# Performance work log

Measured on AMD Instinct MI355X. Metric: run time of the kernel, lower is better.

Reference implementation:

```python
import jax, jax.numpy as jnp
import numpy as np

EPS = 1e-8
N_NODES, N_EDGES = 10000, 160000
SI, VI = 128, 16          # node scalar / vector channels
ES, EV = 32, 4            # edge scalar / vector channels
SO, VO = 128, 16          # output scalar / vector channels
MSI, MVI = 2 * SI + ES, 2 * VI + EV   # message input dims: 288, 36
H1 = max(MVI, VO)         # layer-1 hidden = 36 (bottleneck=1)
H2 = max(VO, VO)          # layer-2 hidden = 16
SVO = 3                   # scalarization_vectorization_output_dim


def _safe_norm(x, axis):
    return jnp.sqrt(jnp.sum(x * x, axis=axis) + EPS)


def _gcp(s, v, frames, Wdown, Wdf, Wso, bso, Wup, Wg, bg):
    """GCP block on edge-level inputs (node_inputs=False, vector_gate=True).
    s: [E, si], v: [E, vi, 3], frames: [E, 3, 3]."""
    v_pre = jnp.swapaxes(v, -1, -2)                 # [E, 3, vi]
    v_hid = v_pre @ Wdown                           # [E, 3, h]
    v_norm = _safe_norm(v_hid, axis=-2)             # [E, h]
    v_frames = v_pre @ Wdf                          # [E, 3, svo]
    # scalarize: frames @ v_frames -> [E,3,svo], transpose -> [E,svo,3], flatten to 9
    local = jnp.swapaxes(frames @ v_frames, -1, -2).reshape(v.shape[0], 3 * SVO)
    merged = jnp.concatenate([s, v_norm, local], axis=-1)
    s_out = merged @ Wso + bso                      # [E, so]
    v_out = jnp.swapaxes(v_hid @ Wup, -1, -2)       # [E, vo, 3]
    gate = jax.nn.sigmoid(jax.nn.silu(s_out) @ Wg + bg)  # vector gate
    v_out = v_out * gate[..., None]
    return jax.nn.silu(s_out), v_out


def _lin(key, fan_in, fan_out):
    return jax.random.normal(key, (fan_in, fan_out), dtype=jnp.float32) / np.sqrt(fan_in)


def setup_inputs() -> dict:
    key = jax.random.key(0)
    ks = jax.random.split(key, 24)
    M1 = H1 + MSI + 3 * SVO   # 333
    M2 = H2 + SO + 3 * SVO    # 153
    return {
        "node_s": jax.random.normal(ks[0], (N_NODES, SI), dtype=jnp.float32),
        "node_v": jax.random.normal(ks[1], (N_NODES, VI, 3), dtype=jnp.float32),
        "edge_s": jax.random.normal(ks[2], (N_EDGES, ES), dtype=jnp.float32),
        "edge_v": jax.random.normal(ks[3], (N_EDGES, EV, 3), dtype=jnp.float32),
        "frames": jax.random.normal(ks[4], (N_EDGES, 3, 3), dtype=jnp.float32),
        "g1_Wdown": _lin(ks[5], MVI, H1),
        "g1_Wdf": _lin(ks[6], MVI, SVO),
        "g1_Wso": _lin(ks[7], M1, SO),
        "g1_bso": jnp.zeros((SO,), dtype=jnp.float32),
        "g1_Wup": _lin(ks[8], H1, VO),
        "g1_Wg": _lin(ks[9], SO, VO),
        "g1_bg": jnp.zeros((VO,), dtype=jnp.float32),
        "g2_Wdown": _lin(ks[10], VO, H2),
        "g2_Wdf": _lin(ks[11], VO, SVO),
        "g2_Wso": _lin(ks[12], M2, SO),
        "g2_bso": jnp.zeros((SO,), dtype=jnp.float32),
        "g2_Wup": _lin(ks[13], H2, VO),
        "g2_Wg": _lin(ks[14], SO, VO),
        "g2_bg": jnp.zeros((VO,), dtype=jnp.float32),
        "att_W": _lin(ks[15], SO, 1),
        "att_b": jnp.zeros((1,), dtype=jnp.float32),
        "edge_index": jax.random.randint(ks[16], (2, N_EDGES), 0, N_NODES, dtype=jnp.int64),
    }


def reference(node_s, node_v, edge_s, edge_v, frames,
              g1_Wdown, g1_Wdf, g1_Wso, g1_bso, g1_Wup, g1_Wg, g1_bg,
              g2_Wdown, g2_Wdf, g2_Wso, g2_bso, g2_Wup, g2_Wg, g2_bg,
              att_W, att_b, edge_index):
    row, col = edge_index[0], edge_index[1]
    # edge gather: concat source node, edge, dest node features
    ms = jnp.concatenate([node_s[row], edge_s, node_s[col]], axis=-1)   # [E, 288]
    mv = jnp.concatenate([node_v[row], edge_v, node_v[col]], axis=1)    # [E, 36, 3]
    # message_fusion[0]
    s, v = _gcp(ms, mv, frames, g1_Wdown, g1_Wdf, g1_Wso, g1_bso, g1_Wup, g1_Wg, g1_bg)
    # message_fusion[1] with residual
    s2, v2 = _gcp(s, v, frames, g2_Wdown, g2_Wdf, g2_Wso, g2_bso, g2_Wup, g2_Wg, g2_bg)
    s, v = s + s2, v + v2
    # scalar message attention
    attn = jax.nn.sigmoid(s @ att_W + att_b)
    s = s * attn
    # flatten ScalarVector and scatter-sum aggregate to destination nodes
    flat = jnp.concatenate([s, v.reshape(v.shape[0], VO * 3)], axis=-1)  # [E, 176]
    agg = jax.ops.segment_sum(flat, row, num_segments=N_NODES)           # [N, 176]
    return agg
```

## Files before the change

### kernel.cpp

```cpp
#include <hip/hip_runtime.h>
#include <hip/hip_bf16.h>

#define E_TOT 160000
#define NN    10000
#define EPB   32

typedef unsigned short ushortT;
typedef unsigned int   uintT;
typedef __attribute__((ext_vector_type(8))) short short8;
typedef __attribute__((ext_vector_type(4))) float f32x4;

__device__ __forceinline__ float sigmoidf_(float x) { return 1.0f / (1.0f + __expf(-x)); }
__device__ __forceinline__ float siluf_(float x) { return x * sigmoidf_(x); }

__device__ __forceinline__ ushortT f2b(float f) {
    union { float f; uintT u; } x; x.f = f;
    uintT r = x.u + 0x7fffu + ((x.u >> 16) & 1u);
    return (ushortT)(r >> 16);
}
__device__ __forceinline__ float b2f(ushortT h) {
    union { uintT u; float f; } x; x.u = ((uintT)h) << 16; return x.f;
}
__device__ __forceinline__ uintT pk2(float lo, float hi) {
    union { __hip_bfloat162 h; uintT u; } cv;
    cv.h = __float22bfloat162_rn(make_float2(lo, hi));
    return cv.u;
}
__device__ __forceinline__ short8 ldfrag(const float* p) {
    const float4 x = ((const float4*)p)[0];
    const float4 y = ((const float4*)p)[1];
    union { uintT u[4]; short8 s; } r;
    r.u[0] = pk2(x.x, x.y); r.u[1] = pk2(x.z, x.w);
    r.u[2] = pk2(y.x, y.y); r.u[3] = pk2(y.z, y.w);
    return r.s;
}

#define OFF_W1SO 0
#define OFF_W2SO 45056
#define OFF_W1DF 65536
#define OFF_W1G  68608
#define OFF_W1UP 70656
#define OFF_W2DF 71680
#define OFF_W2G  72704
#define OFF_W2UP 74752
#define WT_USH   75264

#define NOFF_OFF   56320000ULL
#define CUR_OFF    56360016ULL
#define WT_OFF     57040032ULL
#define WS_CSR     57190560ULL
#define NS16_OFF   57190560ULL
#define WS_NS      59750560ULL
#define PR_OFF     59750560ULL
#define PC_OFF     62310560ULL
#define PRE_END    64870560ULL

__device__ __forceinline__ bool idx_is64(const int* pi) {
    return (pi[1] | pi[3] | pi[5] | pi[7] | pi[9] | pi[11] | pi[13] | pi[15]) == 0;
}

__device__ __forceinline__ void weight_prep(
    int i,
    const float* __restrict__ W1so, const float* __restrict__ W2so,
    const float* __restrict__ W1d,  const float* __restrict__ W1f,
    const float* __restrict__ W1g,  const float* __restrict__ W1up,
    const float* __restrict__ W2d,  const float* __restrict__ W2f,
    const float* __restrict__ W2g,  const float* __restrict__ W2up,
    ushortT* __restrict__ ws)
{
    if (i < OFF_W2SO) {
        int n = i / 352, k = i - n * 352;
        ws[i] = (k < 333) ? f2b(W1so[k * 128 + n]) : (ushortT)0;
    } else if (i < OFF_W1DF) {
        int j = i - OFF_W2SO, n = j / 160, k = j - n * 160;
        ws[i] = (k < 153) ? f2b(W2so[k * 128 + n]) : (ushortT)0;
    } else if (i < OFF_W1G) {
        int j = i - OFF_W1DF, n = j / 64, k = j - n * 64;
        float v = 0.f;
        if (k < 36) { if (n < 36) v = W1d[k * 36 + n]; else if (n < 39) v = W1f[k * 3 + (n - 36)]; }
        ws[i] = f2b(v);
    } else if (i < OFF_W1UP) {
        int j = i - OFF_W1G, n = j / 128, k = j - n * 128;
        ws[i] = f2b(W1g[k * 16 + n]);
    } else if (i < OFF_W2DF) {
        int j = i - OFF_W1UP, n = j / 64, k = j - n * 64;
        ws[i] = (k < 36) ? f2b(W1up[k * 16 + n]) : (ushortT)0;
    } else if (i < OFF_W2G) {
        int j = i - OFF_W2DF, n = j / 32, k = j - n * 32;
        float v = 0.f;
        if (k < 16) { if (n < 16) v = W2d[k * 16 + n]; else if (n < 19) v = W2f[k * 3 + (n - 16)]; }
        ws[i] = f2b(v);
    } else if (i < OFF_W2UP) {
        int j = i - OFF_W2G, n = j / 128, k = j - n * 128;
        ws[i] = f2b(W2g[k * 16 + n]);
    } else if (i < WT_USH) {
        int j = i - OFF_W2UP, n = j / 32, k = j - n * 32;
        ws[i] = (k < 16) ? f2b(W2up[k * 16 + n]) : (ushortT)0;
    }
}

__global__ __launch_bounds__(256) void setup_kernel(
    const float* __restrict__ W1so, const float* __restrict__ W2so,
    const float* __restrict__ W1d,  const float* __restrict__ W1f,
    const float* __restrict__ W1g,  const float* __restrict__ W1up,
    const float* __restrict__ W2d,  const float* __restrict__ W2f,
    const float* __restrict__ W2g,  const float* __restrict__ W2up,
    ushortT* __restrict__ ws,
    const void* __restrict__ eidx, int* __restrict__ cur,
    const float* __restrict__ node_s,
    ushortT* __restrict__ ns16)
{
    int i = blockIdx.x * 256 + threadIdx.x;
    {
        const int* pi = (const int*)eidx;
        const long long* pl = (const long long*)eidx;
        int r = idx_is64(pi) ? (int)pl[i] : pi[i];
        atomicAdd(&cur[r], 1);
    }
    if (ns16 && i < 160000) {
        float4 x = ((const float4*)node_s)[i * 2];
        float4 y = ((const float4*)node_s)[i * 2 + 1];
        uint4 st;
        st.x = pk2(x.x, x.y); st.y = pk2(x.z, x.w);
        st.z = pk2(y.x, y.y); st.w = pk2(y.z, y.w);
        ((uint4*)ns16)[i] = st;
    }
    weight_prep(i, W1so, W2so, W1d, W1f, W1g, W1up, W2d, W2f, W2g, W2up, ws);
}

__global__ __launch_bounds__(256) void prep_kernel(
    const float* __restrict__ W1so, const float* __restrict__ W2so,
    const float* __restrict__ W1d,  const float* __restrict__ W1f,
    const float* __restrict__ W1g,  const float* __restrict__ W1up,
    const float* __restrict__ W2d,  const float* __restrict__ W2f,
    const float* __restrict__ W2g,  const float* __restrict__ W2up,
    ushortT* __restrict__ ws, float* __restrict__ out)
{
    int i = blockIdx.x * 256 + threadIdx.x;
    float4* o4 = (float4*)out;
    #pragma unroll
    for (int k = 0; k < 6; ++k) {
        int z = i + k * 75264;
        if (z < 440000) o4[z] = make_float4(0.f, 0.f, 0.f, 0.f);
    }
    weight_prep(i, W1so, W2so, W1d, W1f, W1g, W1up, W2d, W2f, W2g, W2up, ws);
}

__global__ __launch_bounds__(256) void scan_kernel(int* __restrict__ cur,
                                                   int* __restrict__ noff)
{
    __shared__ int buf[10000];
    __shared__ int partial[256];
    const int t = threadIdx.x;
    for (int i = t; i < NN; i += 256) buf[i] = cur[i];
    for (int i = t; i < NN; i += 256) cur[i] = 0;
    __syncthreads();
    const int base = t * 40;
    int s = 0;
    #pragma unroll
    for (int i = 0; i < 40; ++i) s += (base + i < NN) ? buf[base + i] : 0;
    partial[t] = s;
    __syncthreads();
    for (int o = 1; o < 256; o <<= 1) {
        int v = (t >= o) ? partial[t - o] : 0;
        __syncthreads();
        partial[t] += v;
        __syncthreads();
    }
    int run = (t == 0) ? 0 : partial[t - 1];
    #pragma unroll
    for (int i = 0; i < 40; ++i) {
        int gi = base + i;
        if (gi < NN) { int v = buf[gi]; noff[gi] = run; run += v; }
    }
    if (t == 255) noff[NN] = partial[255];
}

#define MFMA(a, b, c) __builtin_amdgcn_mfma_f32_16x16x32_bf16((a), (b), (c), 0, 0, 0)

__global__ __launch_bounds__(256) void pre_kernel(
    const ushortT* __restrict__ ns16, const ushortT* __restrict__ wt,
    ushortT* __restrict__ prt, ushortT* __restrict__ pct,
    int* __restrict__ cur, int* __restrict__ noff)
{
    __shared__ int sbuf[10000];
    __shared__ int spart[256];
    const int t = threadIdx.x;
    if (blockIdx.x == 625) {
        for (int i = t; i < NN; i += 256) sbuf[i] = cur[i];
        for (int i = t; i < NN; i += 256) cur[i] = 0;
        __syncthreads();
        const int base = t * 40;
        int s = 0;
        #pragma unroll
        for (int i = 0; i < 40; ++i) s += (base + i < NN) ? sbuf[base + i] : 0;
        spart[t] = s;
        __syncthreads();
        for (int o = 1; o < 256; o <<= 1) {
            int v = (t >= o) ? spart[t - o] : 0;
            __syncthreads();
            spart[t] += v;
            __syncthreads();
        }
        int run = (t == 0) ? 0 : spart[t - 1];
        #pragma unroll
        for (int i = 0; i < 40; ++i) {
            int gi = base + i;
            if (gi < NN) { int v = sbuf[gi]; noff[gi] = run; run += v; }
        }
        if (t == 255) noff[NN] = spart[255];
        return;
    }
    const int w = t >> 6, lane = t & 63, lq = lane >> 4, ln = lane & 15, klq = lq * 8;
    const int nb = blockIdx.x * 16;
    const int dn0 = w * 32 + ln, dn1 = dn0 + 16;
    const ushortT* b0p = wt + dn0 * 352 + klq;
    const ushortT* b1p = wt + dn1 * 352 + klq;
    const ushortT* arow = ns16 + (size_t)(nb + ln) * 128 + klq;
    f32x4 a00 = {0,0,0,0}, a01 = {0,0,0,0}, a10 = {0,0,0,0}, a11 = {0,0,0,0};
    #pragma unroll
    for (int ks = 0; ks < 4; ++ks) {
        short8 a  = *(const short8*)(arow + ks * 32);
        short8 b0 = *(const short8*)(b0p + ks * 32);
        short8 b1 = *(const short8*)(b1p + ks * 32);
        short8 c0 = *(const short8*)(b0p + 160 + ks * 32);
        short8 c1 = *(const short8*)(b1p + 160 + ks * 32);
        a00 = MFMA(a, b0, a00); a01 = MFMA(a, b1, a01);
        a10 = MFMA(a, c0, a10); a11 = MFMA(a, c1, a11);
    }
    #pragma unroll
    for (int r = 0; r < 4; ++r) {
        int n = nb + lq * 4 + r;
        prt[(size_t)n * 128 + dn0] = f2b(a00[r]);
        prt[(size_t)n * 128 + dn1] = f2b(a01[r]);
        pct[(size_t)n * 128 + dn0] = f2b(a10[r]);
        pct[(size_t)n * 128 + dn1] = f2b(a11[r]);
    }
}

__global__ __launch_bounds__(256) void node_kernel(const ushortT* __restrict__ fb,
                                                   const int* __restrict__ noff,
                                                   float* __restrict__ out)
{
    const int w = threadIdx.x >> 6, l = threadIdx.x & 63;
    const int n = blockIdx.x * 4 + w;
    if (l >= 44) return;
    const int s = noff[n], eend = noff[n + 1];
    float a0 = 0.f, a1 = 0.f, a2 = 0.f, a3 = 0.f;
    int idx = s;
    for (; idx + 2 <= eend; idx += 2) {
        uint2 p0 = *(const uint2*)(fb + (size_t)idx * 176 + l * 4);
        uint2 p1 = *(const uint2*)(fb + (size_t)(idx + 1) * 176 + l * 4);
        a0 += b2f((ushortT)(p0.x & 0xffff)); a1 += b2f((ushortT)(p0.x >> 16));
        a2 += b2f((ushortT)(p0.y & 0xffff)); a3 += b2f((ushortT)(p0.y >> 16));
        a0 += b2f((ushortT)(p1.x & 0xffff)); a1 += b2f((ushortT)(p1.x >> 16));
        a2 += b2f((ushortT)(p1.y & 0xffff)); a3 += b2f((ushortT)(p1.y >> 16));
    }
    if (idx < eend) {
        uint2 p0 = *(const uint2*)(fb + (size_t)idx * 176 + l * 4);
        a0 += b2f((ushortT)(p0.x & 0xffff)); a1 += b2f((ushortT)(p0.x >> 16));
        a2 += b2f((ushortT)(p0.y & 0xffff)); a3 += b2f((ushortT)(p0.y >> 16));
    }
    ((float4*)(out + (size_t)n * 176))[l] = make_float4(a0, a1, a2, a3);
}

__global__ __launch_bounds__(256, 6) void edge_kernel(
    const float* __restrict__ node_s, const float* __restrict__ node_v,
    const float* __restrict__ edge_s, const float* __restrict__ edge_v,
    const float* __restrict__ frames,
    const float* __restrict__ b1so, const float* __restrict__ b1g,
    const float* __restrict__ b2so, const float* __restrict__ b2g,
    const float* __restrict__ attW, const float* __restrict__ attb,
    const ushortT* __restrict__ wsc,
    const void* __restrict__ eidx, float* __restrict__ out,
    ushortT* __restrict__ fb, int* __restrict__ cur, const int* __restrict__ noff,
    const ushortT* __restrict__ ns16,
    const ushortT* __restrict__ prt, const ushortT* __restrict__ pct,
    int csr)
{
    const ushortT* W1T   = wsc + OFF_W1SO;
    const ushortT* W2T   = wsc + OFF_W2SO;
    const ushortT* W1dfT = wsc + OFF_W1DF;
    const ushortT* W1gT  = wsc + OFF_W1G;
    const ushortT* W1upT = wsc + OFF_W1UP;
    const ushortT* W2dfT = wsc + OFF_W2DF;
    const ushortT* W2gT  = wsc + OFF_W2G;
    const ushortT* W2upT = wsc + OFF_W2UP;

    __shared__ __align__(16) char smem[27136];
    ushortT* mvA     = (ushortT*)smem;
    ushortT* m2      = (ushortT*)smem;
    ushortT* vhidA   = (ushortT*)(smem + 10752);
    ushortT* s2s     = (ushortT*)(smem + 10752);
    ushortT* normbuf = (ushortT*)(smem + 19456);
    ushortT* v1s     = (ushortT*)(smem + 19456);
    ushortT* vhid2A  = (ushortT*)(smem + 19456);
    float*   fr      = (float*)(smem + 24064);
    float*   vfr2f   = (float*)(smem + 25216);
    ushortT* v1f     = (ushortT*)(smem + 24064);

    const int t  = threadIdx.x;
    const int eg = blockIdx.x * EPB;
    const int w  = t >> 6, lane = t & 63, lq = lane >> 4, ln = lane & 15;
    const int te = t >> 3, tj = t & 7;
    const int p  = w & 1;

    const int* pi = (const int*)eidx;
    const long long* pl = (const long long*)eidx;
    const bool is64 = idx_is64(pi);

    int posr = 0;
    float att_reg = 0.f;

    const int nrT = is64 ? (int)pl[eg + te] : pi[eg + te];
    const int ncT = is64 ? (int)pl[E_TOT + eg + te] : pi[E_TOT + eg + te];

    uint4 pga = {0,0,0,0}, pgb = {0,0,0,0}, pgc = {0,0,0,0}, pgd = {0,0,0,0};
    {
        #pragma unroll
        for (int mi = 0; mi < 2; ++mi) {
            if (mi == 1 && tj != 0) break;
            int m = (mi == 0) ? tj : 8;
            const float* src;
            if (m < 4)       src = node_v + nrT * 48 + 12 * m;
            else if (m == 4) src = edge_v + (eg + te) * 12;
            else             src = node_v + ncT * 48 + 12 * (m - 5);
            float4 x = ((const float4*)src)[0];
            float4 y = ((const float4*)src)[1];
            float4 z = ((const float4*)src)[2];
            float v[12] = {x.x, x.y, x.z, x.w, y.x, y.y, y.z, y.w, z.x, z.y, z.z, z.w};
            int c0 = 4 * m;
            #pragma unroll
            for (int sp = 0; sp < 3; ++sp) {
                *(uintT*)(mvA + (sp * 32 + te) * 40 + c0)     = pk2(v[sp],     v[3 + sp]);
                *(uintT*)(mvA + (sp * 32 + te) * 40 + c0 + 2) = pk2(v[6 + sp], v[9 + sp]);
            }
        }
        if (prt) {
            const ushortT* pr_ = prt + (size_t)nrT * 128 + tj * 16;
            const ushortT* pc_ = pct + (size_t)ncT * 128 + tj * 16;
            pga = ((const uint4*)pr_)[0]; pgb = ((const uint4*)pr_)[1];
            pgc = ((const uint4*)pc_)[0]; pgd = ((const uint4*)pc_)[1];
        }
        #pragma unroll
        for (int k = 0; k < 2; ++k) {
            int j = tj + k * 8;
            if (j < 9) fr[te * 9 + j] = frames[(eg + te) * 9 + j];
        }
        #pragma unroll
        for (int k = 0; k < 3; ++k) {
            int c = 45 + tj + k * 8;
            if (c < 64) normbuf[te * 72 + c] = 0;
        }
        if (t < 192) {
            int r = t >> 1, cc = 36 + ((t & 1) << 1);
            *(uintT*)(mvA + r * 40 + cc) = 0;
        }
        if (csr && tj == 0) {
            posr = noff[nrT] + atomicAdd(&cur[nrT], 1);
        }
    }

    const int klq = lq * 8;
    const int dn0 = w * 32 + ln, dn1 = dn0 + 16;
    const ushortT* b0p = W1T + dn0 * 352 + klq;
    const ushortT* b1p = W1T + dn1 * 352 + klq;
    f32x4 acc00 = {0,0,0,0}, acc01 = {0,0,0,0}, acc10 = {0,0,0,0}, acc11 = {0,0,0,0};
    float dbi0, dbi1;
    {
        const int e0 = ln, e1 = 16 + ln;
        const int eb0 = (eg + e0) * 32, eb1 = (eg + e1) * 32;
        dbi0 = b1so[dn0]; dbi1 = b1so[dn1];
        if (prt) {
            short8 a0 = ldfrag(edge_s + eb0 + klq);
            short8 a1 = ldfrag(edge_s + eb1 + klq);
            short8 b0 = *(const short8*)(b0p + 128);
            short8 b1 = *(const short8*)(b1p + 128);
            acc00 = MFMA(a0, b0, acc00); acc01 = MFMA(a0, b1, acc01);
            acc10 = MFMA(a1, b0, acc10); acc11 = MFMA(a1, b1, acc11);
        } else {
            int r0, c0, r1, c1;
            if (is64) {
                r0 = (int)pl[eg + e0]; r1 = (int)pl[eg + e1];
                c0 = (int)pl[E_TOT + eg + e0]; c1 = (int)pl[E_TOT + eg + e1];
            } else {
                r0 = pi[eg + e0]; r1 = pi[eg + e1];
                c0 = pi[E_TOT + eg + e0]; c1 = pi[E_TOT + eg + e1];
            }
            r0 *= 128; c0 *= 128; r1 *= 128; c1 *= 128;
            #pragma unroll
            for (int ks = 0; ks < 9; ++ks) {
                short8 a0, a1;
                if (ks < 4) {
                    if (ns16) {
                        a0 = *(const short8*)(ns16 + r0 + ks * 32 + klq);
                        a1 = *(const short8*)(ns16 + r1 + ks * 32 + klq);
                    } else {
                        a0 = ldfrag(node_s + r0 + ks * 32 + klq);
                        a1 = ldfrag(node_s + r1 + ks * 32 + klq);
                    }
                } else if (ks == 4) {
                    a0 = ldfrag(edge_s + eb0 + klq);
                    a1 = ldfrag(edge_s + eb1 + klq);
                } else {
                    if (ns16) {
                        a0 = *(const short8*)(ns16 + c0 + (ks - 5) * 32 + klq);
                        a1 = *(const short8*)(ns16 + c1 + (ks - 5) * 32 + klq);
                    } else {
                        a0 = ldfrag(node_s + c0 + (ks - 5) * 32 + klq);
                        a1 = ldfrag(node_s + c1 + (ks - 5) * 32 + klq);
                    }
                }
                short8 b0 = *(const short8*)(b0p + ks * 32);
                short8 b1 = *(const short8*)(b1p + ks * 32);
                acc00 = MFMA(a0, b0, acc00); acc01 = MFMA(a0, b1, acc01);
                acc10 = MFMA(a1, b0, acc10); acc11 = MFMA(a1, b1, acc11);
            }
        }
    }
    asm volatile("" : "+v"(acc00), "+v"(acc01), "+v"(acc10), "+v"(acc11));
    __syncthreads();

    for (int u = w; u < 18; u += 4) {
        int mt = u / 3, nt = u - mt * 3;
        const ushortT* ap = mvA + (mt * 16 + ln) * 40 + lq * 8;
        const ushortT* bp = W1dfT + (nt * 16 + ln) * 64 + lq * 8;
        f32x4 acc = {0.f, 0.f, 0.f, 0.f};
        acc = MFMA(*(const short8*)ap, *(const short8*)bp, acc);
        short8 a2 = {0, 0, 0, 0, 0, 0, 0, 0};
        if (lq == 0) a2 = *(const short8*)(ap + 32);
        acc = MFMA(a2, *(const short8*)(bp + 32), acc);
        if (nt < 2 || ln < 8) {
            ushortT* op = vhidA + (mt * 16 + lq * 4) * 40 + nt * 16 + ln;
            op[0]   = f2b(acc[0]); op[40]  = f2b(acc[1]);
            op[80]  = f2b(acc[2]); op[120] = f2b(acc[3]);
        }
    }
    __syncthreads();

    {
        #pragma unroll
        for (int k = 0; k < 5; ++k) {
            int h = tj + k * 8;
            if (h < 36) {
                float a0 = b2f(vhidA[te * 40 + h]);
                float a1 = b2f(vhidA[(32 + te) * 40 + h]);
                float a2 = b2f(vhidA[(64 + te) * 40 + h]);
                normbuf[te * 72 + h] = f2b(sqrtf(fmaf(a0, a0, fmaf(a1, a1, fmaf(a2, a2, 1e-8f)))));
            }
        }
        for (int i = t; i < 288; i += 256) {
            int e = i / 9, r = i - e * 9, a = r / 3, b = r - a * 3;
            float x = fr[e * 9 + b * 3 + 0] * b2f(vhidA[e * 40 + 36 + a])
                    + fr[e * 9 + b * 3 + 1] * b2f(vhidA[(32 + e) * 40 + 36 + a])
                    + fr[e * 9 + b * 3 + 2] * b2f(vhidA[(64 + e) * 40 + 36 + a]);
            normbuf[e * 72 + 36 + r] = f2b(x);
        }
        if (prt) {
            uintT pr_[8] = {pga.x, pga.y, pga.z, pga.w, pgb.x, pgb.y, pgb.z, pgb.w};
            uintT pc_[8] = {pgc.x, pgc.y, pgc.z, pgc.w, pgd.x, pgd.y, pgd.z, pgd.w};
            uintT* dst = (uintT*)(m2 + te * 168 + tj * 16);
            #pragma unroll
            for (int j = 0; j < 8; ++j) {
                float lo = b2f((ushortT)(pr_[j] & 0xffff)) + b2f((ushortT)(pc_[j] & 0xffff));
                float hi = b2f((ushortT)(pr_[j] >> 16))    + b2f((ushortT)(pc_[j] >> 16));
                dst[j] = pk2(lo, hi);
            }
        }
    }
    __syncthreads();

    {
        const int e0 = ln, e1 = 16 + ln;
        #pragma unroll
        for (int ks = 9; ks < 11; ++ks) {
            short8 a0 = *(const short8*)(normbuf + e0 * 72 + (ks - 9) * 32 + klq);
            short8 a1 = *(const short8*)(normbuf + e1 * 72 + (ks - 9) * 32 + klq);
            short8 b0 = *(const short8*)(b0p + ks * 32);
            short8 b1 = *(const short8*)(b1p + ks * 32);
            acc00 = MFMA(a0, b0, acc00); acc01 = MFMA(a0, b1, acc01);
            acc10 = MFMA(a1, b0, acc10); acc11 = MFMA(a1, b1, acc11);
        }
        if (prt) {
            #pragma unroll
            for (int r = 0; r < 4; ++r) {
                int m0 = lq * 4 + r;
                float p00 = b2f(m2[m0 * 168 + dn0]);
                float p01 = b2f(m2[m0 * 168 + dn1]);
                float p10 = b2f(m2[(16 + m0) * 168 + dn0]);
                float p11 = b2f(m2[(16 + m0) * 168 + dn1]);
                m2[m0 * 168 + dn0]        = f2b(siluf_(acc00[r] + p00 + dbi0));
                m2[m0 * 168 + dn1]        = f2b(siluf_(acc01[r] + p01 + dbi1));
                m2[(16 + m0) * 168 + dn0] = f2b(siluf_(acc10[r] + p10 + dbi0));
                m2[(16 + m0) * 168 + dn1] = f2b(siluf_(acc11[r] + p11 + dbi1));
            }
        } else {
            #pragma unroll
            for (int r = 0; r < 4; ++r) {
                int m0 = lq * 4 + r;
                m2[m0 * 168 + dn0]        = f2b(siluf_(acc00[r] + dbi0));
                m2[m0 * 168 + dn1]        = f2b(siluf_(acc01[r] + dbi1));
                m2[(16 + m0) * 168 + dn0] = f2b(siluf_(acc10[r] + dbi0));
                m2[(16 + m0) * 168 + dn1] = f2b(siluf_(acc11[r] + dbi1));
            }
        }
    }
    __syncthreads();

    float v1reg[2][4] = {{0.f,0.f,0.f,0.f},{0.f,0.f,0.f,0.f}};
    {
        f32x4 gacc = {0,0,0,0};
        {
            const ushortT* ap = m2 + (p * 16 + ln) * 168;
            const ushortT* bp = W1gT + ln * 128;
            #pragma unroll
            for (int ks = 0; ks < 4; ++ks)
                gacc = MFMA(*(const short8*)(ap + ks * 32 + lq * 8),
                            *(const short8*)(bp + ks * 32 + lq * 8), gacc);
        }
        float g1[4];
        {
            float bi = b1g[ln];
            #pragma unroll
            for (int r = 0; r < 4; ++r) g1[r] = sigmoidf_(gacc[r] + bi);
        }
        const ushortT* bpu = W1upT + ln * 64 + lq * 8;
        short8 bu1 = *(const short8*)bpu;
        short8 bu2 = *(const short8*)(bpu + 32);
        #pragma unroll
        for (int c = 0; c < 2; ++c) {
            if (c == 1 && w >= 2) break;
            int mt = w + c * 4;
            const ushortT* ap = vhidA + (mt * 16 + ln) * 40 + lq * 8;
            f32x4 acc = {0,0,0,0};
            acc = MFMA(*(const short8*)ap, bu1, acc);
            short8 a2 = {0, 0, 0, 0, 0, 0, 0, 0};
            if (lq == 0) a2 = *(const short8*)(ap + 32);
            acc = MFMA(a2, bu2, acc);
            #pragma unroll
            for (int r = 0; r < 4; ++r) {
                int row = mt * 16 + lq * 4 + r;
                float vv = acc[r] * g1[r];
                v1reg[c][r] = vv;
                v1s[row * 16 + ln] = f2b(vv);
            }
        }
        #pragma unroll
        for (int c = 0; c < 2; ++c) {
            if (c == 1 && w >= 2) break;
            int mt = w + c * 4;
            const ushortT* ap = v1s + (mt * 16 + ln) * 16 + lq * 8;
            short8 a = {0, 0, 0, 0, 0, 0, 0, 0};
            if (lq < 2) a = *(const short8*)ap;
            #pragma unroll
            for (int nt = 0; nt < 2; ++nt) {
                const ushortT* bp = W2dfT + (nt * 16 + ln) * 32 + lq * 8;
                f32x4 acc = {0,0,0,0};
                acc = MFMA(a, *(const short8*)bp, acc);
                if (nt == 0) {
                    ushortT* op = vhid2A + (mt * 16 + lq * 4) * 16 + ln;
                    op[0]  = f2b(acc[0]); op[16] = f2b(acc[1]);
                    op[32] = f2b(acc[2]); op[48] = f2b(acc[3]);
                } else if (ln < 3) {
                    float* op = vfr2f + (mt * 16 + lq * 4) * 3 + ln;
                    op[0] = acc[0]; op[3] = acc[1]; op[6] = acc[2]; op[9] = acc[3];
                }
            }
        }
    }
    __syncthreads();

    {
        #pragma unroll
        for (int k = 0; k < 2; ++k) {
            int i = t + k * 256, e = i >> 4, h = i & 15;
            float a0 = b2f(vhid2A[e * 16 + h]);
            float a1 = b2f(vhid2A[(32 + e) * 16 + h]);
            float a2 = b2f(vhid2A[(64 + e) * 16 + h]);
            m2[e * 168 + 128 + h] = f2b(sqrtf(fmaf(a0, a0, fmaf(a1, a1, fmaf(a2, a2, 1e-8f)))));
        }
        for (int i = t; i < 288; i += 256) {
            int e = i / 9, r = i - e * 9, a = r / 3, b = r - a * 3;
            float x = fr[e * 9 + b * 3 + 0] * vfr2f[e * 3 + a]
                    + fr[e * 9 + b * 3 + 1] * vfr2f[(32 + e) * 3 + a]
                    + fr[e * 9 + b * 3 + 2] * vfr2f[(64 + e) * 3 + a];
            m2[e * 168 + 144 + r] = f2b(x);
        }
        if (tj) m2[te * 168 + 152 + tj] = 0;
    }
    __syncthreads();

    {
        f32x4 acc00i = {0,0,0,0}, acc01i = {0,0,0,0}, acc10i = {0,0,0,0}, acc11i = {0,0,0,0};
        const ushortT* a0p = m2 + ln * 168 + lq * 8;
        const ushortT* a1p = m2 + (16 + ln) * 168 + lq * 8;
        const ushortT* b0pi = W2T + (w * 32 + ln) * 160 + lq * 8;
        const ushortT* b1pi = W2T + (w * 32 + 16 + ln) * 160 + lq * 8;
        #pragma unroll
        for (int ks = 0; ks < 5; ++ks) {
            short8 a0 = *(const short8*)(a0p + ks * 32);
            short8 a1 = *(const short8*)(a1p + ks * 32);
            short8 b0 = *(const short8*)(b0pi + ks * 32);
            short8 b1 = *(const short8*)(b1pi + ks * 32);
            acc00i = MFMA(a0, b0, acc00i); acc01i = MFMA(a0, b1, acc01i);
            acc10i = MFMA(a1, b0, acc10i); acc11i = MFMA(a1, b1, acc11i);
        }
        const int n0 = w * 32 + ln, n1 = n0 + 16;
        float bi0 = b2so[n0], bi1 = b2so[n1];
        #pragma unroll
        for (int r = 0; r < 4; ++r) {
            int m0 = lq * 4 + r;
            s2s[m0 * 136 + n0]        = f2b(siluf_(acc00i[r] + bi0));
            s2s[m0 * 136 + n1]        = f2b(siluf_(acc01i[r] + bi1));
            s2s[(16 + m0) * 136 + n0] = f2b(siluf_(acc10i[r] + bi0));
            s2s[(16 + m0) * 136 + n1] = f2b(siluf_(acc11i[r] + bi1));
        }
    }
    __syncthreads();

    {
        f32x4 gacc = {0,0,0,0};
        {
            const ushortT* ap = s2s + (p * 16 + ln) * 136;
            const ushortT* bp = W2gT + ln * 128;
            #pragma unroll
            for (int ks = 0; ks < 4; ++ks)
                gacc = MFMA(*(const short8*)(ap + ks * 32 + lq * 8),
                            *(const short8*)(bp + ks * 32 + lq * 8), gacc);
        }
        float g2[4];
        {
            float bi = b2g[ln];
            #pragma unroll
            for (int r = 0; r < 4; ++r) g2[r] = sigmoidf_(gacc[r] + bi);
        }
        const ushortT* bpu = W2upT + ln * 32 + lq * 8;
        short8 bu = *(const short8*)bpu;
        #pragma unroll
        for (int c = 0; c < 2; ++c) {
            if (c == 1 && w >= 2) break;
            int mt = w + c * 4;
            const ushortT* ap = vhid2A + (mt * 16 + ln) * 16 + lq * 8;
            short8 a = {0, 0, 0, 0, 0, 0, 0, 0};
            if (lq < 2) a = *(const short8*)ap;
            f32x4 acc = {0,0,0,0};
            acc = MFMA(a, bu, acc);
            #pragma unroll
            for (int r = 0; r < 4; ++r) {
                int row = mt * 16 + lq * 4 + r;
                float vfin = v1reg[c][r] + acc[r] * g2[r];
                v1f[row * 16 + ln] = f2b(vfin);
            }
        }
        {
            float sum = 0.f;
            int c0 = tj * 16;
            #pragma unroll
            for (int c = c0; c < c0 + 16; ++c)
                sum = fmaf(b2f(m2[te * 168 + c]) + b2f(s2s[te * 136 + c]), attW[c], sum);
            sum += __shfl_xor(sum, 4);
            sum += __shfl_xor(sum, 2);
            sum += __shfl_xor(sum, 1);
            att_reg = sigmoidf_(sum + attb[0]);
        }
    }
    __syncthreads();

    {
        const float at = att_reg;
        if (csr) {
            const int pos = __shfl(posr, lane & 56);
            ushortT* fbe = fb + (size_t)pos * 176;
            #pragma unroll
            for (int k = 0; k < 11; ++k) {
                int j = 2 * tj + 16 * k;
                float v0, v1;
                if (j < 128) {
                    v0 = (b2f(m2[te * 168 + j])     + b2f(s2s[te * 136 + j]))     * at;
                    v1 = (b2f(m2[te * 168 + j + 1]) + b2f(s2s[te * 136 + j + 1])) * at;
                } else {
                    int r = j - 128;
                    int o0 = r / 3,        sp0 = r - o0 * 3;
                    int o1 = (r + 1) / 3,  sp1 = (r + 1) - o1 * 3;
                    v0 = b2f(v1f[(sp0 * 32 + te) * 16 + o0]);
                    v1 = b2f(v1f[(sp1 * 32 + te) * 16 + o1]);
                }
                *(uintT*)(fbe + j) = pk2(v0, v1);
            }
        } else {
            const int orow = nrT * 176;
            #pragma unroll
            for (int k = 0; k < 22; ++k) {
                int j = tj + k * 8;
                float val;
                if (j < 128) {
                    val = (b2f(m2[te * 168 + j]) + b2f(s2s[te * 136 + j])) * at;
                } else {
                    int r = j - 128, o = r / 3, sp = r - o * 3;
                    val = b2f(v1f[(sp * 32 + te) * 16 + o]);
                }
                atomicAdd(&out[orow + j], val);
            }
        }
    }
}

extern "C" void kernel_launch(void* const* d_in, const int* in_sizes, int n_in,
                              void* d_out, int out_size, void* d_ws, size_t ws_size,
                              hipStream_t stream) {
    const float* node_s = (const float*)d_in[0];
    const float* node_v = (const float*)d_in[1];
    const float* edge_s = (const float*)d_in[2];
    const float* edge_v = (const float*)d_in[3];
    const float* frames = (const float*)d_in[4];
    const float* W1d  = (const float*)d_in[5];
    const float* W1f  = (const float*)d_in[6];
    const float* W1so = (const float*)d_in[7];
    const float* b1so = (const float*)d_in[8];
    const float* W1up = (const float*)d_in[9];
    const float* W1g  = (const float*)d_in[10];
    const float* b1g  = (const float*)d_in[11];
    const float* W2d  = (const float*)d_in[12];
    const float* W2f  = (const float*)d_in[13];
    const float* W2so = (const float*)d_in[14];
    const float* b2so = (const float*)d_in[15];
    const float* W2up = (const float*)d_in[16];
    const float* W2g  = (const float*)d_in[17];
    const float* b2g  = (const float*)d_in[18];
    const float* attW = (const float*)d_in[19];
    const float* attb = (const float*)d_in[20];
    const void*  eidx = d_in[21];

    float* out = (float*)d_out;
    char* ws = (char*)d_ws;

    const int csr = ws_size >= WS_CSR;
    ushortT* wt    = csr ? (ushortT*)(ws + WT_OFF)  : (ushortT*)ws;
    ushortT* fbuf  = csr ? (ushortT*)ws             : nullptr;
    int*     noff  = csr ? (int*)(ws + NOFF_OFF)    : nullptr;
    int*     cur   = csr ? (int*)(ws + CUR_OFF)     : nullptr;
    ushortT* ns16  = (ws_size >= WS_NS) ? (ushortT*)(ws + NS16_OFF) : nullptr;
    const int pre  = csr && ns16 && (ws_size >= PRE_END);
    ushortT* prt   = pre ? (ushortT*)(ws + PR_OFF) : nullptr;
    ushortT* pct   = pre ? (ushortT*)(ws + PC_OFF) : nullptr;

    if (csr) {
        hipMemsetAsync(cur, 0, NN * sizeof(int), stream);
        setup_kernel<<<625, 256, 0, stream>>>(
            W1so, W2so, W1d, W1f, W1g, W1up, W2d, W2f, W2g, W2up,
            wt, eidx, cur, node_s, ns16);
        if (pre) {
            pre_kernel<<<626, 256, 0, stream>>>(ns16, wt, prt, pct, cur, noff);
        } else {
            scan_kernel<<<1, 256, 0, stream>>>(cur, noff);
        }
    } else {
        prep_kernel<<<294, 256, 0, stream>>>(W1so, W2so, W1d, W1f, W1g, W1up,
                                             W2d, W2f, W2g, W2up, wt, out);
    }

    edge_kernel<<<E_TOT / EPB, 256, 0, stream>>>(
        node_s, node_v, edge_s, edge_v, frames,
        b1so, b1g, b2so, b2g, attW, attb,
        (const ushortT*)wt, eidx, out, fbuf, cur, noff, ns16, prt, pct, csr);

    if (csr) {
        node_kernel<<<2500, 256, 0, stream>>>((const ushortT*)fbuf, noff, out);
    }
}
```

Baseline: 277.8 us.

## Fold node pre-projection into setup kernel and drop bf16 node copy

The per-node projection of node_s through the W1so row and column blocks now runs in extra blocks of setup_kernel. Those blocks load node_s fp32 directly and stage a swizzled bf16 weight tile in shared memory, so the separate ns16 conversion buffer and pre_kernel launch go away. The scan moves back to its own single-block kernel. Separately, node_kernel's gather loop is unrolled from 2 to 4 edges. This trades one launch and an intermediate buffer for per-block weight staging in the setup blocks and a serial scan launch.

```diff
diff --git a/kernel.cpp b/kernel.cpp
--- a/kernel.cpp
+++ b/kernel.cpp
@@ -49,11 +49,9 @@
 #define CUR_OFF    56360016ULL
 #define WT_OFF     57040032ULL
 #define WS_CSR     57190560ULL
-#define NS16_OFF   57190560ULL
-#define WS_NS      59750560ULL
-#define PR_OFF     59750560ULL
-#define PC_OFF     62310560ULL
-#define PRE_END    64870560ULL
+#define PR_OFF     57190560ULL
+#define PC_OFF     59750560ULL
+#define PRE_END    62310560ULL
 
 __device__ __forceinline__ bool idx_is64(const int* pi) {
     return (pi[1] | pi[3] | pi[5] | pi[7] | pi[9] | pi[11] | pi[13] | pi[15]) == 0;
@@ -99,6 +97,8 @@
     }
 }
 
+#define MFMA(a, b, c) __builtin_amdgcn_mfma_f32_16x16x32_bf16((a), (b), (c), 0, 0, 0)
+
 __global__ __launch_bounds__(256) void setup_kernel(
     const float* __restrict__ W1so, const float* __restrict__ W2so,
     const float* __restrict__ W1d,  const float* __restrict__ W1f,
@@ -108,22 +108,58 @@
     ushortT* __restrict__ ws,
     const void* __restrict__ eidx, int* __restrict__ cur,
     const float* __restrict__ node_s,
-    ushortT* __restrict__ ns16)
+    ushortT* __restrict__ prt, ushortT* __restrict__ pct)
 {
-    int i = blockIdx.x * 256 + threadIdx.x;
+    __shared__ __align__(16) ushortT wtile[128 * 128];
+    const int t = threadIdx.x;
+
+    if (blockIdx.x >= 625) {
+        if (!prt) return;
+        const int nb = (blockIdx.x - 625) * 64;
+        const int w = t >> 6, lane = t & 63, lq = lane >> 4, ln = lane & 15, klq = lq * 8;
+        int arow = nb + w * 16 + ln;
+        if (arow > NN - 1) arow = NN - 1;
+        short8 af[4];
+        #pragma unroll
+        for (int ks = 0; ks < 4; ++ks)
+            af[ks] = ldfrag(node_s + (size_t)arow * 128 + ks * 32 + klq);
+        const int n_ = t & 127, half = t >> 7, nsw8 = n_ & 7;
+        for (int pass = 0; pass < 2; ++pass) {
+            const int base = pass ? 160 : 0;
+            for (int kk = 0; kk < 64; ++kk) {
+                int kt = kk * 2 + half;
+                float v = W1so[(base + kt) * 128 + n_];
+                wtile[n_ * 128 + ((((kt >> 3) ^ nsw8) << 3) | (kt & 7))] = f2b(v);
+            }
+            __syncthreads();
+            ushortT* dst = pass ? pct : prt;
+            #pragma unroll
+            for (int ct = 0; ct < 8; ++ct) {
+                f32x4 ar = {0, 0, 0, 0};
+                const int n = ct * 16 + ln, nsw = n & 7;
+                #pragma unroll
+                for (int ks = 0; ks < 4; ++ks) {
+                    const int kb = ks * 32 + klq;
+                    const short8 br = *(const short8*)(wtile + n * 128 + (((kb >> 3) ^ nsw) << 3));
+                    ar = MFMA(af[ks], br, ar);
+                }
+                #pragma unroll
+                for (int r = 0; r < 4; ++r) {
+                    const int node = nb + w * 16 + lq * 4 + r;
+                    if (node < NN) dst[(size_t)node * 128 + ct * 16 + ln] = f2b(ar[r]);
+                }
+            }
+            __syncthreads();
+        }
+        return;
+    }
+
+    int i = blockIdx.x * 256 + t;
     {
         const int* pi = (const int*)eidx;
         const long long* pl = (const long long*)eidx;
         int r = idx_is64(pi) ? (int)pl[i] : pi[i];
         atomicAdd(&cur[r], 1);
-    }
-    if (ns16 && i < 160000) {
-        float4 x = ((const float4*)node_s)[i * 2];
-        float4 y = ((const float4*)node_s)[i * 2 + 1];
-        uint4 st;
-        st.x = pk2(x.x, x.y); st.y = pk2(x.z, x.w);
-        st.z = pk2(y.x, y.y); st.w = pk2(y.z, y.w);
-        ((uint4*)ns16)[i] = st;
     }
     weight_prep(i, W1so, W2so, W1d, W1f, W1g, W1up, W2d, W2f, W2g, W2up, ws);
 }
@@ -176,68 +212,6 @@
     if (t == 255) noff[NN] = partial[255];
 }
 
-#define MFMA(a, b, c) __builtin_amdgcn_mfma_f32_16x16x32_bf16((a), (b), (c), 0, 0, 0)
-
-__global__ __launch_bounds__(256) void pre_kernel(
-    const ushortT* __restrict__ ns16, const ushortT* __restrict__ wt,
-    ushortT* __restrict__ prt, ushortT* __restrict__ pct,
-    int* __restrict__ cur, int* __restrict__ noff)
-{
-    __shared__ int sbuf[10000];
-    __shared__ int spart[256];
-    const int t = threadIdx.x;
-    if (blockIdx.x == 625) {
-        for (int i = t; i < NN; i += 256) sbuf[i] = cur[i];
-        for (int i = t; i < NN; i += 256) cur[i] = 0;
-        __syncthreads();
-        const int base = t * 40;
-        int s = 0;
-        #pragma unroll
-        for (int i = 0; i < 40; ++i) s += (base + i < NN) ? sbuf[base + i] : 0;
-        spart[t] = s;
-        __syncthreads();
-        for (int o = 1; o < 256; o <<= 1) {
-            int v = (t >= o) ? spart[t - o] : 0;
-            __syncthreads();
-            spart[t] += v;
-            __syncthreads();
-        }
-        int run = (t == 0) ? 0 : spart[t - 1];
-        #pragma unroll
-        for (int i = 0; i < 40; ++i) {
-            int gi = base + i;
-            if (gi < NN) { int v = sbuf[gi]; noff[gi] = run; run += v; }
-        }
-        if (t == 255) noff[NN] = spart[255];
-        return;
-    }
-    const int w = t >> 6, lane = t & 63, lq = lane >> 4, ln = lane & 15, klq = lq * 8;
-    const int nb = blockIdx.x * 16;
-    const int dn0 = w * 32 + ln, dn1 = dn0 + 16;
-    const ushortT* b0p = wt + dn0 * 352 + klq;
-    const ushortT* b1p = wt + dn1 * 352 + klq;
-    const ushortT* arow = ns16 + (size_t)(nb + ln) * 128 + klq;
-    f32x4 a00 = {0,0,0,0}, a01 = {0,0,0,0}, a10 = {0,0,0,0}, a11 = {0,0,0,0};
-    #pragma unroll
-    for (int ks = 0; ks < 4; ++ks) {
-        short8 a  = *(const short8*)(arow + ks * 32);
-        short8 b0 = *(const short8*)(b0p + ks * 32);
-        short8 b1 = *(const short8*)(b1p + ks * 32);
-        short8 c0 = *(const short8*)(b0p + 160 + ks * 32);
-        short8 c1 = *(const short8*)(b1p + 160 + ks * 32);
-        a00 = MFMA(a, b0, a00); a01 = MFMA(a, b1, a01);
-        a10 = MFMA(a, c0, a10); a11 = MFMA(a, c1, a11);
-    }
-    #pragma unroll
-    for (int r = 0; r < 4; ++r) {
-        int n = nb + lq * 4 + r;
-        prt[(size_t)n * 128 + dn0] = f2b(a00[r]);
-        prt[(size_t)n * 128 + dn1] = f2b(a01[r]);
-        pct[(size_t)n * 128 + dn0] = f2b(a10[r]);
-        pct[(size_t)n * 128 + dn1] = f2b(a11[r]);
-    }
-}
-
 __global__ __launch_bounds__(256) void node_kernel(const ushortT* __restrict__ fb,
                                                    const int* __restrict__ noff,
                                                    float* __restrict__ out)
@@ -248,15 +222,21 @@
     const int s = noff[n], eend = noff[n + 1];
     float a0 = 0.f, a1 = 0.f, a2 = 0.f, a3 = 0.f;
     int idx = s;
-    for (; idx + 2 <= eend; idx += 2) {
+    for (; idx + 4 <= eend; idx += 4) {
         uint2 p0 = *(const uint2*)(fb + (size_t)idx * 176 + l * 4);
         uint2 p1 = *(const uint2*)(fb + (size_t)(idx + 1) * 176 + l * 4);
+        uint2 p2 = *(const uint2*)(fb + (size_t)(idx + 2) * 176 + l * 4);
+        uint2 p3 = *(const uint2*)(fb + (size_t)(idx + 3) * 176 + l * 4);
         a0 += b2f((ushortT)(p0.x & 0xffff)); a1 += b2f((ushortT)(p0.x >> 16));
         a2 += b2f((ushortT)(p0.y & 0xffff)); a3 += b2f((ushortT)(p0.y >> 16));
         a0 += b2f((ushortT)(p1.x & 0xffff)); a1 += b2f((ushortT)(p1.x >> 16));
         a2 += b2f((ushortT)(p1.y & 0xffff)); a3 += b2f((ushortT)(p1.y >> 16));
-    }
-    if (idx < eend) {
+        a0 += b2f((ushortT)(p2.x & 0xffff)); a1 += b2f((ushortT)(p2.x >> 16));
+        a2 += b2f((ushortT)(p2.y & 0xffff)); a3 += b2f((ushortT)(p2.y >> 16));
+        a0 += b2f((ushortT)(p3.x & 0xffff)); a1 += b2f((ushortT)(p3.x >> 16));
+        a2 += b2f((ushortT)(p3.y & 0xffff)); a3 += b2f((ushortT)(p3.y >> 16));
+    }
+    for (; idx < eend; ++idx) {
         uint2 p0 = *(const uint2*)(fb + (size_t)idx * 176 + l * 4);
         a0 += b2f((ushortT)(p0.x & 0xffff)); a1 += b2f((ushortT)(p0.x >> 16));
         a2 += b2f((ushortT)(p0.y & 0xffff)); a3 += b2f((ushortT)(p0.y >> 16));
@@ -392,24 +372,14 @@
             for (int ks = 0; ks < 9; ++ks) {
                 short8 a0, a1;
                 if (ks < 4) {
-                    if (ns16) {
-                        a0 = *(const short8*)(ns16 + r0 + ks * 32 + klq);
-                        a1 = *(const short8*)(ns16 + r1 + ks * 32 + klq);
-                    } else {
-                        a0 = ldfrag(node_s + r0 + ks * 32 + klq);
-                        a1 = ldfrag(node_s + r1 + ks * 32 + klq);
-                    }
+                    a0 = ldfrag(node_s + r0 + ks * 32 + klq);
+                    a1 = ldfrag(node_s + r1 + ks * 32 + klq);
                 } else if (ks == 4) {
                     a0 = ldfrag(edge_s + eb0 + klq);
                     a1 = ldfrag(edge_s + eb1 + klq);
                 } else {
-                    if (ns16) {
-                        a0 = *(const short8*)(ns16 + c0 + (ks - 5) * 32 + klq);
-                        a1 = *(const short8*)(ns16 + c1 + (ks - 5) * 32 + klq);
-                    } else {
-                        a0 = ldfrag(node_s + c0 + (ks - 5) * 32 + klq);
-                        a1 = ldfrag(node_s + c1 + (ks - 5) * 32 + klq);
-                    }
+                    a0 = ldfrag(node_s + c0 + (ks - 5) * 32 + klq);
+                    a1 = ldfrag(node_s + c1 + (ks - 5) * 32 + klq);
                 }
                 short8 b0 = *(const short8*)(b0p + ks * 32);
                 short8 b1 = *(const short8*)(b1p + ks * 32);
@@ -739,21 +709,16 @@
     ushortT* fbuf  = csr ? (ushortT*)ws             : nullptr;
     int*     noff  = csr ? (int*)(ws + NOFF_OFF)    : nullptr;
     int*     cur   = csr ? (int*)(ws + CUR_OFF)     : nullptr;
-    ushortT* ns16  = (ws_size >= WS_NS) ? (ushortT*)(ws + NS16_OFF) : nullptr;
-    const int pre  = csr && ns16 && (ws_size >= PRE_END);
+    const int pre  = csr && (ws_size >= PRE_END);
     ushortT* prt   = pre ? (ushortT*)(ws + PR_OFF) : nullptr;
     ushortT* pct   = pre ? (ushortT*)(ws + PC_OFF) : nullptr;
 
     if (csr) {
         hipMemsetAsync(cur, 0, NN * sizeof(int), stream);
-        setup_kernel<<<625, 256, 0, stream>>>(
+        setup_kernel<<<pre ? 782 : 625, 256, 0, stream>>>(
             W1so, W2so, W1d, W1f, W1g, W1up, W2d, W2f, W2g, W2up,
-            wt, eidx, cur, node_s, ns16);
-        if (pre) {
-            pre_kernel<<<626, 256, 0, stream>>>(ns16, wt, prt, pct, cur, noff);
-        } else {
-            scan_kernel<<<1, 256, 0, stream>>>(cur, noff);
-        }
+            wt, eidx, cur, node_s, prt, pct);
+        scan_kernel<<<1, 256, 0, stream>>>(cur, noff);
     } else {
         prep_kernel<<<294, 256, 0, stream>>>(W1so, W2so, W1d, W1f, W1g, W1up,
                                              W2d, W2f, W2g, W2up, wt, out);
@@ -762,7 +727,8 @@
     edge_kernel<<<E_TOT / EPB, 256, 0, stream>>>(
         node_s, node_v, edge_s, edge_v, frames,
         b1so, b1g, b2so, b2g, attW, attb,
-        (const ushortT*)wt, eidx, out, fbuf, cur, noff, ns16, prt, pct, csr);
+        (const ushortT*)wt, eidx, out, fbuf, cur, noff,
+        nullptr, prt, pct, csr);
 
     if (csr) {
         node_kernel<<<2500, 256, 0, stream>>>((const ushortT*)fbuf, noff, out);
```

After: 271.7 us, median of 3. -2.2%, faster.
